# Performance work log

Measured on AMD Instinct MI355X. Metric: run time of the kernel, lower is better.

Reference implementation:

```python
import jax, jax.numpy as jnp
import numpy as np

RES = 128
SIGMA = 2
EPS = 1e-6
# 8 corner combinations of a voxel, [8, 3], static numpy constant
COMBOS = np.stack(np.meshgrid(*[[0, 1]] * 3, indexing='ij'), axis=-1).reshape(8, 3)


def _corner_idx_weights(points, res):
    """Trilinear corner indices and weights.
    points: [B, N, 3] in [0,1). Returns idx [B,N,8,3] int32, w [B,N,8].
    Matches torch code: weight for a corner = prod over dims of distance to
    the OPPOSITE corner coordinate, divided by voxel size.
    """
    pr = points * res
    lo = jnp.floor(pr)
    li = lo.astype(jnp.int32) % res           # lower index (mod res)
    ui = jnp.ceil(pr).astype(jnp.int32) % res  # upper index (mod res)
    frac = pr - lo                             # fractional offset in voxel
    c = COMBOS[None, None]                     # [1,1,8,3]
    idx = jnp.where(c == 1, ui[:, :, None, :], li[:, :, None, :])   # [B,N,8,3]
    wd = jnp.where(c == 1, frac[:, :, None, :], 1.0 - frac[:, :, None, :])
    w = jnp.prod(wd, axis=-1)                  # [B,N,8]
    return idx, w


def point_rasterization(points, features, res):
    """Scatter-add trilinear splatting. Returns [B, F, res, res, res]."""
    B, N, _ = points.shape
    F = features.shape[2]
    idx, w = _corner_idx_weights(points, res)
    vals = w[..., None] * features[:, :, None, :]          # [B,N,8,F]
    flat = (idx[..., 0] * res + idx[..., 1]) * res + idx[..., 2]  # [B,N,8]

    def scat(fl, v):  # fl [N,8], v [N,8,F]
        g = jnp.zeros((res * res * res, F), dtype=v.dtype)
        g = g.at[fl.reshape(-1)].add(v.reshape(-1, F))
        return g.T.reshape(F, res, res, res)

    return jax.vmap(scat)(flat, vals)


def grid_interpolation(field, points, res):
    """Trilinear gather. field: [B, res, res, res], points: [B,N,3] -> [B,N]."""
    idx, w = _corner_idx_weights(points, res)

    def gath(f, ix):  # f [res,res,res], ix [N,8,3]
        return f[ix[..., 0], ix[..., 1], ix[..., 2]]  # [N,8]

    vals = jax.vmap(gath)(field, idx)  # [B,N,8]
    return jnp.sum(w * vals, axis=-1)  # [B,N]


def _fft_freq_grid(res):
    f = jnp.fft.fftfreq(res, d=1.0 / res).astype(jnp.float32)  # integer frequencies
    return jnp.stack(jnp.meshgrid(f, f, f, indexing='ij'), axis=-1)  # [res,res,res,3]


def setup_inputs() -> dict:
    key = jax.random.key(0)
    k1, k2 = jax.random.split(key)
    points = jax.random.uniform(k1, (1, 250000, 3), dtype=jnp.float32) * 0.999
    normals = jax.random.normal(k2, (1, 250000, 3), dtype=jnp.float32)
    return {"points": points, "normals": normals}


def reference(points, normals):
    res = RES
    u = _fft_freq_grid(res)                                  # [X,Y,Z,3]
    u_sq = jnp.sum(u ** 2, axis=-1)                          # [X,Y,Z]
    g = jnp.exp(-2.0 * (SIGMA / res) ** 2 * u_sq)            # gaussian smoothing

    v = point_rasterization(points, normals, res)            # [B,3,X,Y,Z]
    v_tilde = jnp.fft.fftn(v, axes=(2, 3, 4)).transpose(0, 2, 3, 4, 1)  # [B,X,Y,Z,3]

    vec = jnp.sum(u[None] * v_tilde, axis=-1) / (u_sq[None] + EPS)      # [B,X,Y,Z]
    chi_tilde = g[None] * ((-1j / (2 * jnp.pi)) * vec)
    chi_prime = jnp.fft.ifftn(chi_tilde, axes=(1, 2, 3)).real            # [B,X,Y,Z]

    chi_c = grid_interpolation(chi_prime, points, res)        # [B,N]
    vecf = chi_prime - jnp.mean(chi_c, axis=-1)[:, None, None, None]
    chi_0 = vecf[:, 0, 0, 0]                                  # [B]
    chi = (0.5 / jnp.abs(chi_0))[:, None, None, None] * vecf
    return chi
```

## Files before the change

kernel.cpp:

```cpp
#include <hip/hip_runtime.h>
#include <math.h>

#define RES 128
#define RES2 (RES*RES)
#define RES3 (RES*RES*RES)
#define NROWS 16384
#define STRIPW 32

__device__ __forceinline__ int brev7(unsigned x){ return (int)(__brev(x) >> 25); }
__device__ __forceinline__ float freq_of(int s){ int k = brev7((unsigned)s); return (float)(k < 64 ? k : k - 128); }
__device__ __forceinline__ float2 cmul(float2 a, float2 b){
    return make_float2(a.x*b.x - a.y*b.y, a.x*b.y + a.y*b.x);
}
__device__ __forceinline__ float2 twd(float ang){ float s, c; __sincosf(ang, &s, &c); return make_float2(c, s); }

struct TW { float2 s64; float2 w[6]; };
__device__ __forceinline__ TW make_tw(int tt){
    TW t;
    t.s64 = twd(-(float)M_PI * (float)tt * (1.f/64.f));
    #pragma unroll
    for (int i = 0; i < 6; i++){
        int h = 32 >> i;
        t.w[i] = twd(-(float)M_PI * (float)(tt & (h - 1)) / (float)h);
    }
    return t;
}

__device__ __forceinline__ void dif128_t(float2& r0, float2& r1, int tt, const TW& tw){
    {
        float2 a = r0, b = r1;
        r0 = make_float2(a.x + b.x, a.y + b.y);
        float2 d = make_float2(a.x - b.x, a.y - b.y);
        r1 = cmul(d, tw.s64);
    }
    #pragma unroll
    for (int i = 0; i < 6; i++){
        int h = 32 >> i;
        int bit = tt & h;
        float2 w = tw.w[i];
        float2 o0 = make_float2(__shfl_xor(r0.x, h), __shfl_xor(r0.y, h));
        float2 o1 = make_float2(__shfl_xor(r1.x, h), __shfl_xor(r1.y, h));
        if (!bit){
            r0.x += o0.x; r0.y += o0.y;
            r1.x += o1.x; r1.y += o1.y;
        } else {
            r0 = cmul(make_float2(o0.x - r0.x, o0.y - r0.y), w);
            r1 = cmul(make_float2(o1.x - r1.x, o1.y - r1.y), w);
        }
    }
}

__device__ __forceinline__ void dit128_t(float2& r0, float2& r1, int tt, const TW& tw){
    #pragma unroll
    for (int i = 5; i >= 0; i--){
        int h = 32 >> i;
        int bit = tt & h;
        float2 w = make_float2(tw.w[i].x, -tw.w[i].y);
        float2 o0 = make_float2(__shfl_xor(r0.x, h), __shfl_xor(r0.y, h));
        float2 o1 = make_float2(__shfl_xor(r1.x, h), __shfl_xor(r1.y, h));
        if (!bit){
            float2 t0 = cmul(o0, w), t1 = cmul(o1, w);
            r0.x += t0.x; r0.y += t0.y;
            r1.x += t1.x; r1.y += t1.y;
        } else {
            float2 t0 = cmul(r0, w), t1 = cmul(r1, w);
            r0 = make_float2(o0.x - t0.x, o0.y - t0.y);
            r1 = make_float2(o1.x - t1.x, o1.y - t1.y);
        }
    }
    {
        float2 w = make_float2(tw.s64.x, -tw.s64.y);
        float2 b = cmul(r1, w);
        float2 a = r0;
        r0 = make_float2(a.x + b.x, a.y + b.y);
        r1 = make_float2(a.x - b.x, a.y - b.y);
    }
}

__global__ void hist_kernel(const float* __restrict__ pts, int* __restrict__ counts, int N){
    int i = blockIdx.x * blockDim.x + threadIdx.x;
    if (i >= N) return;
    float prx = pts[3*i] * RES, pry = pts[3*i+1] * RES;
    int lx = ((int)floorf(prx)) & 127, ly = ((int)floorf(pry)) & 127;
    atomicAdd(&counts[(lx << 7) | ly], 1);
}

__global__ __launch_bounds__(1024) void rowscan(const int* __restrict__ counts,
                                                int* __restrict__ starts,
                                                int* __restrict__ cursors){
    __shared__ int buf[2][1024];
    int t = threadIdx.x;
    int c[16];
    int base = t * 16;
    int s = 0;
    #pragma unroll
    for (int k = 0; k < 16; k++){ c[k] = counts[base + k]; s += c[k]; }
    buf[0][t] = s;
    __syncthreads();
    int cur = 0;
    for (int d = 1; d < 1024; d <<= 1){
        int v = buf[cur][t];
        if (t >= d) v += buf[cur][t - d];
        buf[cur ^ 1][t] = v;
        cur ^= 1;
        __syncthreads();
    }
    int incl = buf[cur][t];
    int run = incl - s;
    #pragma unroll
    for (int k = 0; k < 16; k++){ starts[base + k] = run; cursors[base + k] = run; run += c[k]; }
    if (t == 1023) starts[NROWS] = incl;
}

__global__ void scatter_sorted(const float* __restrict__ pts, const float* __restrict__ nrm,
                               int* __restrict__ cursors, float4* __restrict__ sorted4, int N){
    int i = blockIdx.x * blockDim.x + threadIdx.x;
    if (i >= N) return;
    float px = pts[3*i], py = pts[3*i+1], pz = pts[3*i+2];
    int lx = ((int)floorf(px * RES)) & 127, ly = ((int)floorf(py * RES)) & 127;
    int pos = atomicAdd(&cursors[(lx << 7) | ly], 1);
    sorted4[2*pos]     = make_float4(px, py, pz, nrm[3*i]);
    sorted4[2*pos + 1] = make_float4(nrm[3*i+1], nrm[3*i+2], 0.f, 0.f);
}

__global__ __launch_bounds__(768) void gather_z(const float4* __restrict__ sorted4,
                                                const int* __restrict__ starts,
                                                float2* __restrict__ zF){
    __shared__ float col[3][STRIPW][RES];
    int x  = blockIdx.x >> 2;
    int y0 = (blockIdx.x & 3) << 5;
    int t = threadIdx.x;
    #pragma unroll
    for (int k = 0; k < 16; k++) ((float*)col)[t + 768*k] = 0.f;
    __syncthreads();
    int xm = (x + 127) & 127;
    int ybase = (y0 == 0) ? 127 : (y0 - 1);
    int n1 = (y0 == 0) ? 1 : 33;
    int n2 = 33 - n1;
    int a_s[4], a_e[4];
    { int r = (xm << 7) | ybase; a_s[0] = starts[r]; a_e[0] = starts[r + n1]; }
    { int r = (xm << 7);         a_s[1] = starts[r]; a_e[1] = starts[r + n2]; }
    { int r = (x  << 7) | ybase; a_s[2] = starts[r]; a_e[2] = starts[r + n1]; }
    { int r = (x  << 7);         a_s[3] = starts[r]; a_e[3] = starts[r + n2]; }
    int p1 = a_e[0] - a_s[0];
    int p2 = p1 + (a_e[1] - a_s[1]);
    int p3 = p2 + (a_e[2] - a_s[2]);
    int tot = p3 + (a_e[3] - a_s[3]);
    for (int base = 0; base < tot; base += 768){
        int k = base + t;
        if (k < tot){
            int i;
            if      (k < p1) i = a_s[0] + k;
            else if (k < p2) i = a_s[1] + (k - p1);
            else if (k < p3) i = a_s[2] + (k - p2);
            else             i = a_s[3] + (k - p3);
            float4 qa = sorted4[2*i];
            float4 qb = sorted4[2*i + 1];
            float prx = qa.x*RES, pry = qa.y*RES, prz = qa.z*RES;
            float flx = floorf(prx), fly = floorf(pry), flz = floorf(prz);
            float fx = prx - flx, fy = pry - fly, fz = prz - flz;
            int lxp = ((int)flx) & 127, lyp = ((int)fly) & 127, lz = ((int)flz) & 127;
            float wx = (lxp == x) ? (1.f - fx) : fx;
            int z1 = (lz + 1) & 127;
            float n0 = qa.w, nv1 = qb.x, nv2 = qb.y;
            int jA = (lyp - y0) & 127;
            int jB = (jA + 1) & 127;
            if (jA < STRIPW){
                float wy = wx * (1.f - fy);
                float w0 = wy * (1.f - fz), w1 = wy * fz;
                atomicAdd(&col[0][jA][lz], w0*n0);  atomicAdd(&col[0][jA][z1], w1*n0);
                atomicAdd(&col[1][jA][lz], w0*nv1); atomicAdd(&col[1][jA][z1], w1*nv1);
                atomicAdd(&col[2][jA][lz], w0*nv2); atomicAdd(&col[2][jA][z1], w1*nv2);
            }
            if (jB < STRIPW){
                float wy = wx * fy;
                float w0 = wy * (1.f - fz), w1 = wy * fz;
                atomicAdd(&col[0][jB][lz], w0*n0);  atomicAdd(&col[0][jB][z1], w1*n0);
                atomicAdd(&col[1][jB][lz], w0*nv1); atomicAdd(&col[1][jB][z1], w1*nv1);
                atomicAdd(&col[2][jB][lz], w0*nv2); atomicAdd(&col[2][jB][z1], w1*nv2);
            }
        }
    }
    __syncthreads();
    int w = t >> 6, tt = t & 63;
    TW tw = make_tw(tt);
    #pragma unroll
    for (int r = 0; r < 8; r++){
        int idx = r * 12 + w;
        int c = idx >> 5, j = idx & 31;
        float2 r0 = make_float2(col[c][j][tt], 0.f);
        float2 r1 = make_float2(col[c][j][tt + 64], 0.f);
        dif128_t(r0, r1, tt, tw);
        float2* qo = zF + (size_t)c * RES3 + (((size_t)x << 14) | ((size_t)(y0 + j) << 7));
        qo[tt] = r0; qo[tt + 64] = r1;
    }
}

__global__ __launch_bounds__(1024) void mega_y(const float2* __restrict__ zF,
                                               float2* __restrict__ bufA,
                                               float2* __restrict__ bufB){
    __shared__ float2 tile[16][130];
    int t = threadIdx.x;
    int x = blockIdx.x >> 3, z0 = (blockIdx.x & 7) << 4;
    size_t base = ((size_t)x << 14) + (size_t)z0;
    int yv = t >> 3;
    int z2 = (t & 7) << 1;
    size_t gi = base + ((size_t)yv << 7) + z2;
    const float4* zF4 = (const float4*)zF;
    float4 L1 = zF4[((size_t)RES3 + gi) >> 1];
    float4 L2 = zF4[(2*(size_t)RES3 + gi) >> 1];
    float4 L0 = zF4[gi >> 1];
    int w = t >> 6, tt = t & 63;
    TW tw = make_tw(tt);
    tile[z2][yv] = make_float2(L1.x, L1.y); tile[z2+1][yv] = make_float2(L1.z, L1.w);
    __syncthreads();
    float2 A0 = tile[w][tt], A1 = tile[w][tt + 64];
    __syncthreads();
    dif128_t(A0, A1, tt, tw);
    { float f0 = freq_of(tt), f1 = freq_of(tt + 64);
      A0.x *= f0; A0.y *= f0; A1.x *= f1; A1.y *= f1; }
    tile[z2][yv] = make_float2(L2.x, L2.y); tile[z2+1][yv] = make_float2(L2.z, L2.w);
    __syncthreads();
    float2 C0 = tile[w][tt], C1 = tile[w][tt + 64];
    __syncthreads();
    dif128_t(C0, C1, tt, tw);
    { float fz = freq_of(z0 + w);
      A0.x += fz*C0.x; A0.y += fz*C0.y; A1.x += fz*C1.x; A1.y += fz*C1.y; }
    tile[z2][yv] = make_float2(L0.x, L0.y); tile[z2+1][yv] = make_float2(L0.z, L0.w);
    __syncthreads();
    float2 B0 = tile[w][tt], B1 = tile[w][tt + 64];
    __syncthreads();
    dif128_t(B0, B1, tt, tw);
    tile[w][tt] = A0; tile[w][tt + 64] = A1;
    __syncthreads();
    { float2 a = tile[z2][yv], b = tile[z2+1][yv];
      ((float4*)bufA)[gi >> 1] = make_float4(a.x, a.y, b.x, b.y); }
    __syncthreads();
    tile[w][tt] = B0; tile[w][tt + 64] = B1;
    __syncthreads();
    { float2 a = tile[z2][yv], b = tile[z2+1][yv];
      ((float4*)bufB)[gi >> 1] = make_float4(a.x, a.y, b.x, b.y); }
}

__global__ __launch_bounds__(1024) void x_mega(const float2* __restrict__ bufB,
                                               float2* __restrict__ bufA){
    __shared__ float2 tA[16][130];
    __shared__ float2 tB[16][130];
    int t = threadIdx.x;
    int y = blockIdx.x >> 3, z0 = (blockIdx.x & 7) << 4;
    size_t base = ((size_t)y << 7) + (size_t)z0;
    int xv = t >> 3, z2 = (t & 7) << 1;
    size_t gi = base + ((size_t)xv << 14) + z2;
    float4 LA = ((const float4*)bufA)[gi >> 1];
    float4 LB = ((const float4*)bufB)[gi >> 1];
    tA[z2][xv] = make_float2(LA.x, LA.y); tA[z2+1][xv] = make_float2(LA.z, LA.w);
    tB[z2][xv] = make_float2(LB.x, LB.y); tB[z2+1][xv] = make_float2(LB.z, LB.w);
    __syncthreads();
    int w = t >> 6, tt = t & 63;
    TW tw = make_tw(tt);
    float2 a0 = tA[w][tt], a1 = tA[w][tt + 64];
    float2 b0 = tB[w][tt], b1 = tB[w][tt + 64];
    dif128_t(a0, a1, tt, tw);
    dif128_t(b0, b1, tt, tw);
    float fy = freq_of(y), fz = freq_of(z0 + w);
    float fyz = fy*fy + fz*fz;
    const float K = -2.f * (2.f/128.f) * (2.f/128.f);
    {
        float fx = freq_of(tt);
        float vx = a0.x + fx*b0.x, vy = a0.y + fx*b0.y;
        float usq = fx*fx + fyz;
        float s = __expf(K*usq) / ((usq + 1e-6f) * (2.f*(float)M_PI));
        a0 = make_float2(s*vy, -s*vx);
    }
    {
        float fx = freq_of(tt + 64);
        float vx = a1.x + fx*b1.x, vy = a1.y + fx*b1.y;
        float usq = fx*fx + fyz;
        float s = __expf(K*usq) / ((usq + 1e-6f) * (2.f*(float)M_PI));
        a1 = make_float2(s*vy, -s*vx);
    }
    dit128_t(a0, a1, tt, tw);
    tA[w][tt] = a0; tA[w][tt + 64] = a1;
    __syncthreads();
    { float2 a = tA[z2][xv], b = tA[z2+1][xv];
      ((float4*)bufA)[gi >> 1] = make_float4(a.x, a.y, b.x, b.y); }
}

__global__ __launch_bounds__(1024) void inv_y(float2* __restrict__ data){
    __shared__ float2 tile[16][130];
    int t = threadIdx.x;
    int x = blockIdx.x >> 3, z0 = (blockIdx.x & 7) << 4;
    size_t base = ((size_t)x << 14) + (size_t)z0;
    int yv = t >> 3, z2 = (t & 7) << 1;
    size_t gi = base + ((size_t)yv << 7) + z2;
    float4 L = ((const float4*)data)[gi >> 1];
    tile[z2][yv] = make_float2(L.x, L.y); tile[z2+1][yv] = make_float2(L.z, L.w);
    __syncthreads();
    int w = t >> 6, tt = t & 63;
    TW tw = make_tw(tt);
    float2 r0 = tile[w][tt], r1 = tile[w][tt + 64];
    dit128_t(r0, r1, tt, tw);
    tile[w][tt] = r0; tile[w][tt + 64] = r1;
    __syncthreads();
    { float2 a = tile[z2][yv], b = tile[z2+1][yv];
      ((float4*)data)[gi >> 1] = make_float4(a.x, a.y, b.x, b.y); }
}

__global__ __launch_bounds__(256) void inv_z_c2r(const float2* __restrict__ in, float* __restrict__ out){
    int t = threadIdx.x; int wid = t >> 6, tt = t & 63;
    size_t line = (size_t)blockIdx.x * 4 + wid;
    const float2* p = in + line * RES;
    TW tw = make_tw(tt);
    float2 r0 = p[tt], r1 = p[tt + 64];
    dit128_t(r0, r1, tt, tw);
    const float sc = 1.f / (float)RES3;
    float* q = out + line * RES;
    q[tt] = r0.x * sc; q[tt + 64] = r1.x * sc;
}

__global__ void interp_sum(const float* __restrict__ chi, const float* __restrict__ pts,
                           float* __restrict__ sum, int N){
    int i = blockIdx.x * blockDim.x + threadIdx.x;
    float val = 0.f;
    if (i < N){
        float px = pts[3*i], py = pts[3*i+1], pz = pts[3*i+2];
        float prx = px * RES, pry = py * RES, prz = pz * RES;
        float lox = floorf(prx), loy = floorf(pry), loz = floorf(prz);
        int lix = ((int)lox) & 127, liy = ((int)loy) & 127, liz = ((int)loz) & 127;
        int uix = ((int)ceilf(prx)) & 127, uiy = ((int)ceilf(pry)) & 127, uiz = ((int)ceilf(prz)) & 127;
        float fx = prx - lox, fy = pry - loy, fz = prz - loz;
        #pragma unroll
        for (int cx = 0; cx < 2; cx++){
            int ix = cx ? uix : lix;
            float wx = cx ? fx : 1.f - fx;
            #pragma unroll
            for (int cy = 0; cy < 2; cy++){
                int iy = cy ? uiy : liy;
                float wxy = wx * (cy ? fy : 1.f - fy);
                #pragma unroll
                for (int cz = 0; cz < 2; cz++){
                    int iz = cz ? uiz : liz;
                    float w = wxy * (cz ? fz : 1.f - fz);
                    val += w * chi[(ix << 14) + (iy << 7) + iz];
                }
            }
        }
    }
    __shared__ float red[256];
    int tid = threadIdx.x;
    red[tid] = val;
    __syncthreads();
    #pragma unroll
    for (int s2 = 128; s2 > 0; s2 >>= 1){
        if (tid < s2) red[tid] += red[tid + s2];
        __syncthreads();
    }
    if (tid == 0) atomicAdd(sum, red[0]);
}

__global__ void final_scale(const float* __restrict__ chi, const float* __restrict__ sum,
                            float* __restrict__ out, float invN){
    int i = blockIdx.x * blockDim.x + threadIdx.x;
    if (i >= RES3) return;
    float mean = sum[0] * invN;
    float sc = 0.5f / fabsf(chi[0] - mean);
    out[i] = sc * (chi[i] - mean);
}

extern "C" void kernel_launch(void* const* d_in, const int* in_sizes, int n_in,
                              void* d_out, int out_size, void* d_ws, size_t ws_size,
                              hipStream_t stream) {
    const float* points  = (const float*)d_in[0];
    const float* normals = (const float*)d_in[1];
    float* out = (float*)d_out;
    char* ws = (char*)d_ws;

    size_t off = 0;
    float2* zF     = (float2*)(ws + off); off += (size_t)3*RES3*8;
    float2* bufA   = (float2*)(ws + off); off += (size_t)RES3*8;
    float2* bufB   = (float2*)(ws + off); off += (size_t)RES3*8;
    float*  chiP   = (float*) (ws + off); off += (size_t)RES3*4;
    float*  sumb   = (float*) (ws + off); off += 64;
    int*    counts = (int*)   (ws + off); off += (size_t)NROWS*4;
    int*    starts = (int*)   (ws + off); off += (size_t)(NROWS+1)*4;
    int*    cursors= (int*)   (ws + off); off += (size_t)NROWS*4;
    off = (off + 15) & ~(size_t)15;
    float4* sorted4 = (float4*)(ws + off);

    int N = in_sizes[0] / 3;

    hipMemsetAsync(counts, 0, (size_t)NROWS*4, stream);
    hipMemsetAsync(sumb, 0, 16, stream);

    hist_kernel<<<(N + 255)/256, 256, 0, stream>>>(points, counts, N);
    rowscan<<<1, 1024, 0, stream>>>(counts, starts, cursors);
    scatter_sorted<<<(N + 255)/256, 256, 0, stream>>>(points, normals, cursors, sorted4, N);
    gather_z<<<128*4, 768, 0, stream>>>(sorted4, starts, zF);

    mega_y<<<1024, 1024, 0, stream>>>(zF, bufA, bufB);
    x_mega<<<1024, 1024, 0, stream>>>(bufB, bufA);
    inv_y<<<1024, 1024, 0, stream>>>(bufA);
    inv_z_c2r<<<RES2/4, 256, 0, stream>>>(bufA, chiP);

    interp_sum<<<(N + 255)/256, 256, 0, stream>>>(chiP, points, sumb, N);
    final_scale<<<RES3/256, 256, 0, stream>>>(chiP, sumb, out, 1.0f / (float)N);
}
```

Measured before the change: 232.0 us.

## Exploit real-input Hermitian symmetry to keep only half the z-spectrum

The rasterized grid is real, so after the z-axis FFT only 64 frequency bins are stored. The y and x passes and the spectral filter now process half the data with half the blocks. The inverse z pass rebuilds the full spectrum from the conjugate symmetry before the c2r transform. This halves the intermediate buffer traffic and FFT work. The Nyquist bin is zeroed on reconstruction, which differs slightly from the reference at that frequency.

New measurement: 213.8 us. 7.8% less time.

```diff
diff --git a/kernel.cpp b/kernel.cpp
--- a/kernel.cpp
+++ b/kernel.cpp
@@ -4,6 +4,7 @@
 #define RES 128
 #define RES2 (RES*RES)
 #define RES3 (RES*RES*RES)
+#define KZ 64
 #define NROWS 16384
 #define STRIPW 32
 
@@ -184,6 +185,7 @@
     __syncthreads();
     int w = t >> 6, tt = t & 63;
     TW tw = make_tw(tt);
+    int k0 = brev7(tt);
     #pragma unroll
     for (int r = 0; r < 8; r++){
         int idx = r * 12 + w;
@@ -191,8 +193,10 @@
         float2 r0 = make_float2(col[c][j][tt], 0.f);
         float2 r1 = make_float2(col[c][j][tt + 64], 0.f);
         dif128_t(r0, r1, tt, tw);
-        float2* qo = zF + (size_t)c * RES3 + (((size_t)x << 14) | ((size_t)(y0 + j) << 7));
-        qo[tt] = r0; qo[tt + 64] = r1;
+        if (k0 < KZ){
+            size_t line = ((size_t)c * 16384 + ((size_t)x << 7) + (y0 + j));
+            ((float4*)(zF + line * KZ))[k0 >> 1] = make_float4(r0.x, r0.y, r1.x, r1.y);
+        }
     }
 }
 
@@ -200,15 +204,15 @@
                                                float2* __restrict__ bufA,
                                                float2* __restrict__ bufB){
     __shared__ float2 tile[16][130];
-    int t = threadIdx.x;
-    int x = blockIdx.x >> 3, z0 = (blockIdx.x & 7) << 4;
-    size_t base = ((size_t)x << 14) + (size_t)z0;
+    const size_t PL = (size_t)16384 * KZ;
+    int t = threadIdx.x;
+    int x = blockIdx.x >> 2, z0 = (blockIdx.x & 3) << 4;
     int yv = t >> 3;
     int z2 = (t & 7) << 1;
-    size_t gi = base + ((size_t)yv << 7) + z2;
+    size_t gi = (((size_t)x << 7) + yv) * KZ + z0 + z2;
     const float4* zF4 = (const float4*)zF;
-    float4 L1 = zF4[((size_t)RES3 + gi) >> 1];
-    float4 L2 = zF4[(2*(size_t)RES3 + gi) >> 1];
+    float4 L1 = zF4[(PL + gi) >> 1];
+    float4 L2 = zF4[(2*PL + gi) >> 1];
     float4 L0 = zF4[gi >> 1];
     int w = t >> 6, tt = t & 63;
     TW tw = make_tw(tt);
@@ -224,7 +228,7 @@
     float2 C0 = tile[w][tt], C1 = tile[w][tt + 64];
     __syncthreads();
     dif128_t(C0, C1, tt, tw);
-    { float fz = freq_of(z0 + w);
+    { float fz = (float)(z0 + w);
       A0.x += fz*C0.x; A0.y += fz*C0.y; A1.x += fz*C1.x; A1.y += fz*C1.y; }
     tile[z2][yv] = make_float2(L0.x, L0.y); tile[z2+1][yv] = make_float2(L0.z, L0.w);
     __syncthreads();
@@ -247,10 +251,9 @@
     __shared__ float2 tA[16][130];
     __shared__ float2 tB[16][130];
     int t = threadIdx.x;
-    int y = blockIdx.x >> 3, z0 = (blockIdx.x & 7) << 4;
-    size_t base = ((size_t)y << 7) + (size_t)z0;
+    int y = blockIdx.x >> 2, z0 = (blockIdx.x & 3) << 4;
     int xv = t >> 3, z2 = (t & 7) << 1;
-    size_t gi = base + ((size_t)xv << 14) + z2;
+    size_t gi = (((size_t)xv << 7) + y) * KZ + z0 + z2;
     float4 LA = ((const float4*)bufA)[gi >> 1];
     float4 LB = ((const float4*)bufB)[gi >> 1];
     tA[z2][xv] = make_float2(LA.x, LA.y); tA[z2+1][xv] = make_float2(LA.z, LA.w);
@@ -262,7 +265,7 @@
     float2 b0 = tB[w][tt], b1 = tB[w][tt + 64];
     dif128_t(a0, a1, tt, tw);
     dif128_t(b0, b1, tt, tw);
-    float fy = freq_of(y), fz = freq_of(z0 + w);
+    float fy = freq_of(y), fz = (float)(z0 + w);
     float fyz = fy*fy + fz*fz;
     const float K = -2.f * (2.f/128.f) * (2.f/128.f);
     {
@@ -289,10 +292,9 @@
 __global__ __launch_bounds__(1024) void inv_y(float2* __restrict__ data){
     __shared__ float2 tile[16][130];
     int t = threadIdx.x;
-    int x = blockIdx.x >> 3, z0 = (blockIdx.x & 7) << 4;
-    size_t base = ((size_t)x << 14) + (size_t)z0;
+    int x = blockIdx.x >> 2, z0 = (blockIdx.x & 3) << 4;
     int yv = t >> 3, z2 = (t & 7) << 1;
-    size_t gi = base + ((size_t)yv << 7) + z2;
+    size_t gi = (((size_t)x << 7) + yv) * KZ + z0 + z2;
     float4 L = ((const float4*)data)[gi >> 1];
     tile[z2][yv] = make_float2(L.x, L.y); tile[z2+1][yv] = make_float2(L.z, L.w);
     __syncthreads();
@@ -307,14 +309,25 @@
 }
 
 __global__ __launch_bounds__(256) void inv_z_c2r(const float2* __restrict__ in, float* __restrict__ out){
-    int t = threadIdx.x; int wid = t >> 6, tt = t & 63;
-    size_t line = (size_t)blockIdx.x * 4 + wid;
-    const float2* p = in + line * RES;
+    __shared__ float2 ld[4 * KZ];
+    int t = threadIdx.x;
+    int wid = t >> 6, tt = t & 63;
+    size_t blk = (size_t)blockIdx.x;
+    ld[t] = in[blk * (4*KZ) + t];
+    __syncthreads();
+    const float2* D = ld + wid * KZ;
+    int k0 = brev7(tt);
+    int k1 = k0 + 1;
+    float2 r0, r1;
+    if (k0 < KZ)        r0 = D[k0];
+    else if (k0 == 64)  r0 = make_float2(0.f, 0.f);
+    else                { float2 v = D[128 - k0]; r0 = make_float2(v.x, -v.y); }
+    if (k1 < KZ)        r1 = D[k1];
+    else                { float2 v = D[128 - k1]; r1 = make_float2(v.x, -v.y); }
     TW tw = make_tw(tt);
-    float2 r0 = p[tt], r1 = p[tt + 64];
     dit128_t(r0, r1, tt, tw);
     const float sc = 1.f / (float)RES3;
-    float* q = out + line * RES;
+    float* q = out + (blk * 4 + wid) * RES;
     q[tt] = r0.x * sc; q[tt + 64] = r1.x * sc;
 }
 
@@ -376,9 +389,9 @@
     char* ws = (char*)d_ws;
 
     size_t off = 0;
-    float2* zF     = (float2*)(ws + off); off += (size_t)3*RES3*8;
-    float2* bufA   = (float2*)(ws + off); off += (size_t)RES3*8;
-    float2* bufB   = (float2*)(ws + off); off += (size_t)RES3*8;
+    float2* zF     = (float2*)(ws + off); off += (size_t)3*RES2*KZ*8;
+    float2* bufA   = (float2*)(ws + off); off += (size_t)RES2*KZ*8;
+    float2* bufB   = (float2*)(ws + off); off += (size_t)RES2*KZ*8;
     float*  chiP   = (float*) (ws + off); off += (size_t)RES3*4;
     float*  sumb   = (float*) (ws + off); off += 64;
     int*    counts = (int*)   (ws + off); off += (size_t)NROWS*4;
@@ -397,9 +410,9 @@
     scatter_sorted<<<(N + 255)/256, 256, 0, stream>>>(points, normals, cursors, sorted4, N);
     gather_z<<<128*4, 768, 0, stream>>>(sorted4, starts, zF);
 
-    mega_y<<<1024, 1024, 0, stream>>>(zF, bufA, bufB);
-    x_mega<<<1024, 1024, 0, stream>>>(bufB, bufA);
-    inv_y<<<1024, 1024, 0, stream>>>(bufA);
+    mega_y<<<512, 1024, 0, stream>>>(zF, bufA, bufB);
+    x_mega<<<512, 1024, 0, stream>>>(bufB, bufA);
+    inv_y<<<512, 1024, 0, stream>>>(bufA);
     inv_z_c2r<<<RES2/4, 256, 0, stream>>>(bufA, chiP);
 
     interp_sum<<<(N + 255)/256, 256, 0, stream>>>(chiP, points, sumb, N);
```
